# Kernel optimization log

Measured on AMD Instinct MI355X. Metric: run time of the kernel, lower is better.

## Reference

```python
import jax, jax.numpy as jnp
import numpy as np
from functools import partial

NODES = 50
IN_SZ = 12
HID = 6


def _conv(x, W, b):
    # x: [N, C, H, W], W: [O, I, 3, 3], pad 1 -> same H, W
    y = jax.lax.conv_general_dilated(x, W, window_strides=(1, 1),
                                     padding=((1, 1), (1, 1)),
                                     dimension_numbers=('NCHW', 'OIHW', 'NCHW'))
    return y + b[None, :, None, None]


def setup_inputs() -> dict:
    key = jax.random.key(0)
    ks = jax.random.split(key, 12)
    B, T = 4096, 12
    d = {}
    d['A_hat'] = jax.random.normal(ks[0], (NODES, NODES), dtype=jnp.float32)
    d['X'] = jax.random.normal(ks[1], (B, NODES, T, IN_SZ, 1), dtype=jnp.float32)
    s_ih = 1.0 / np.sqrt(HID)
    d['W_ih'] = jax.random.uniform(ks[2], (4 * HID, IN_SZ), jnp.float32, -s_ih, s_ih)
    d['W_hh'] = jax.random.uniform(ks[3], (4 * HID, HID), jnp.float32, -s_ih, s_ih)
    d['b_ih'] = jax.random.uniform(ks[4], (4 * HID,), jnp.float32, -s_ih, s_ih)
    d['b_hh'] = jax.random.uniform(ks[5], (4 * HID,), jnp.float32, -s_ih, s_ih)
    d['Wf1'] = jax.random.normal(ks[6], (100, 50, 3, 3), jnp.float32) * 0.05
    d['bf1'] = jnp.zeros((100,), jnp.float32)
    d['Wf2'] = jax.random.normal(ks[7], (100, 100, 3, 3), jnp.float32) * 0.05
    d['bf2'] = jnp.zeros((100,), jnp.float32)
    d['Wf3'] = jax.random.normal(ks[8], (50, 100, 3, 3), jnp.float32) * 0.05
    d['bf3'] = jnp.zeros((50,), jnp.float32)
    d['W_lean'] = jax.random.normal(ks[9], (HID, HID), jnp.float32) * 0.3
    d['b_lean'] = jnp.zeros((HID,), jnp.float32)
    return d


def reference(A_hat, X, W_ih, W_hh, b_ih, b_hh, Wf1, bf1, Wf2, bf2, Wf3, bf3, W_lean, b_lean):
    # out1: [S, 50, 12] with S = B*T; the Python loop over S becomes a scan
    out1 = jnp.squeeze(X, axis=4).reshape(-1, NODES, IN_SZ)

    def step(carry, x_t):
        h, c = carry  # each [50, 6]
        gates = x_t @ W_ih.T + b_ih + h @ W_hh.T + b_hh  # [50, 24]
        i, f, g, o = jnp.split(gates, 4, axis=-1)
        i = jax.nn.sigmoid(i)
        f = jax.nn.sigmoid(f)
        g = jnp.tanh(g)
        o = jax.nn.sigmoid(o)
        c_new = f * c + i * g
        h_new = o * jnp.tanh(c_new)
        h_new = jnp.tanh(h_new)  # module applies extra tanh and feeds it back
        return (h_new, c_new), h_new

    h0 = jnp.zeros((NODES, HID), dtype=X.dtype)
    c0 = jnp.zeros((NODES, HID), dtype=X.dtype)
    _, al = jax.lax.scan(step, (h0, c0), out1)  # al: [S, 50, 6]

    out2 = al.reshape(-1, NODES, HID, 1)  # [S, 50, 6, 1]
    f = jax.nn.relu(_conv(out2, Wf1, bf1))
    f = jax.nn.relu(_conv(f, Wf2, bf2))
    f = jax.nn.relu(_conv(f, Wf3, bf3))
    out = (f.reshape(-1, HID) @ W_lean.T + b_lean).reshape(-1, NODES, HID, 1)
    return out
```

## Files before the change

kernel.cpp:

```cpp
#include <hip/hip_runtime.h>

#define NCH 1024
#define CL 48
#define WM 24

typedef _Float16 half8 __attribute__((ext_vector_type(8)));
typedef float f32x4 __attribute__((ext_vector_type(4)));

#define ROWB 256
#define BUFB 17408

__device__ __forceinline__ int swz(int srow, int b){ return srow*ROWB + (b ^ ((srow&7)<<4)); }

__device__ __forceinline__ unsigned short f2h_bits(float x){
  _Float16 h = (_Float16)x;
  return __builtin_bit_cast(unsigned short, h);
}

__device__ __forceinline__ float rcp_(float x){ return __builtin_amdgcn_rcpf(x); }
__device__ __forceinline__ float tanh_(float z){ return 1.f - 2.f*rcp_(1.f + __expf(2.f*z)); }

__global__ void pack_frags(const float* __restrict__ W1, const float* __restrict__ W2,
                           const float* __restrict__ W3, unsigned short* __restrict__ ws)
{
  int tid = blockIdx.x*256 + threadIdx.x;
  if (tid >= 174*512) return;
  int f = tid >> 9, e = tid & 511, l = e >> 3, j = e & 7;
  int d, ks, nt, I, O; const float* W;
  if (f < 42)      { int x = f;     int st = x/7;  nt = x%7; d = st/2; ks = st%2; I = 50;  O = 100; W = W1; }
  else if (f < 126){ int x = f-42;  int st = x/7;  nt = x%7; d = st/4; ks = st%4; I = 100; O = 100; W = W2; }
  else             { int x = f-126; int st = x/4;  nt = x%4; d = st/4; ks = st%4; I = 100; O = 50;  W = W3; }
  int k = ks*32 + ((l>>4)<<3) + j;
  int o = nt*16 + (l&15);
  float v = (k < I && o < O) ? W[((o*I + k)*3 + d)*3 + 1] : 0.f;
  ws[tid] = f2h_bits(v);
}

__global__ __launch_bounds__(64,3) void lstm_scan(
    const float* __restrict__ X, const float* __restrict__ Wih,
    const float* __restrict__ Whh, const float* __restrict__ bih,
    const float* __restrict__ bhh, float* __restrict__ al)
{
  const int l = threadIdx.x;
  const int blk = blockIdx.x;
  const int chunk = blk / 5, w = blk - chunk*5;
  const int q = l / 6, j = l - q*6;
  const bool active = (q < 10);
  const int n = w*10 + (active ? q : 0);
  const int sbase = active ? q*6 : 0;

  const int s_begin = chunk * CL;
  const int s_start = (s_begin >= WM) ? (s_begin - WM) : 0;
  const int s_end   = s_begin + CL;

  float wi[4][12], wh[4][6], bb[4];
  #pragma unroll
  for (int g=0; g<4; ++g){
    const int r = g*6 + j;
    const float4 w0 = *(const float4*)(Wih + r*12);
    const float4 w1 = *(const float4*)(Wih + r*12 + 4);
    const float4 w2 = *(const float4*)(Wih + r*12 + 8);
    wi[g][0]=w0.x; wi[g][1]=w0.y; wi[g][2]=w0.z; wi[g][3]=w0.w;
    wi[g][4]=w1.x; wi[g][5]=w1.y; wi[g][6]=w1.z; wi[g][7]=w1.w;
    wi[g][8]=w2.x; wi[g][9]=w2.y; wi[g][10]=w2.z; wi[g][11]=w2.w;
    const float2 h0 = *(const float2*)(Whh + r*6);
    const float2 h1 = *(const float2*)(Whh + r*6 + 2);
    const float2 h2 = *(const float2*)(Whh + r*6 + 4);
    wh[g][0]=h0.x; wh[g][1]=h0.y; wh[g][2]=h1.x;
    wh[g][3]=h1.y; wh[g][4]=h2.x; wh[g][5]=h2.y;
    bb[g] = bih[r] + bhh[r];
  }

  float h[6];
  #pragma unroll
  for (int k=0;k<6;++k) h[k] = 0.f;
  float c = 0.f;

  const float* xp = X + (size_t)s_start*600 + n*12;
  float4 xa = ((const float4*)xp)[0];
  float4 xb = ((const float4*)xp)[1];
  float4 xc = ((const float4*)xp)[2];

  for (int s = s_start; s < s_end; ++s){
    const float xr[12] = {xa.x,xa.y,xa.z,xa.w, xb.x,xb.y,xb.z,xb.w,
                          xc.x,xc.y,xc.z,xc.w};
    const int sn = (s+1 < s_end) ? (s+1) : s;
    const float* xq = X + (size_t)sn*600 + n*12;
    const float4 ya = ((const float4*)xq)[0];
    const float4 yb = ((const float4*)xq)[1];
    const float4 yc = ((const float4*)xq)[2];

    float a0 = bb[0], a1 = bb[1], a2 = bb[2], a3 = bb[3];
    #pragma unroll
    for (int k=0;k<12;++k){
      a0 += wi[0][k]*xr[k]; a1 += wi[1][k]*xr[k];
      a2 += wi[2][k]*xr[k]; a3 += wi[3][k]*xr[k];
    }
    #pragma unroll
    for (int k=0;k<6;++k){
      a0 += wh[0][k]*h[k]; a1 += wh[1][k]*h[k];
      a2 += wh[2][k]*h[k]; a3 += wh[3][k]*h[k];
    }
    const float gi = rcp_(1.f + __expf(-a0));
    const float gf = rcp_(1.f + __expf(-a1));
    const float gg = 2.f*rcp_(1.f + __expf(-(a2+a2))) - 1.f;
    const float go = rcp_(1.f + __expf(-a3));
    c = gf*c + gi*gg;
    const float hn = tanh_(go * tanh_(c));

    if (active && s >= s_begin) al[(size_t)s*300 + n*6 + j] = hn;

    #pragma unroll
    for (int k=0;k<6;++k) h[k] = __shfl(hn, sbase + k, 64);

    xa = ya; xb = yb; xc = yc;
  }
}

template<int KS, int NTT, int NTG, bool LAST>
__device__ __forceinline__ void conv_layer2(
    char* lds, int inOff, int outOff, const unsigned short* __restrict__ wsU,
    int fbase, int ntOff, const float* __restrict__ bias, int O, int m0, int lane)
{
  f32x4 acc[2][NTG];
  #pragma unroll
  for (int m=0;m<2;m++)
    #pragma unroll
    for (int n=0;n<NTG;n++) acc[m][n] = (f32x4){0.f,0.f,0.f,0.f};

  const int ar = m0 + (lane & 15);
  const int abyte_g = (lane>>4)<<4;
  const int laneb = lane << 3;

  half8 a0c = *(const half8*)(lds + inOff + swz(ar, abyte_g));
  half8 a1c = *(const half8*)(lds + inOff + swz(ar + 16, abyte_g));
  half8 bc[NTG];
  {
    const unsigned short* p0 = wsU + (size_t)(fbase + ntOff)*512 + laneb;
    #pragma unroll
    for (int n=0;n<NTG;n++) bc[n] = *(const half8*)(p0 + n*512);
  }

  #pragma unroll
  for (int st=0; st<3*KS; ++st){
    half8 a0n, a1n, bn[NTG];
    if (st+1 < 3*KS){
      const int dn = (st+1)/KS, ksn = (st+1)%KS;
      a0n = *(const half8*)(lds + inOff + swz(ar + dn, ksn*64 + abyte_g));
      a1n = *(const half8*)(lds + inOff + swz(ar + 16 + dn, ksn*64 + abyte_g));
      const unsigned short* pn = wsU + (size_t)(fbase + (st+1)*NTT + ntOff)*512 + laneb;
      #pragma unroll
      for (int n=0;n<NTG;n++) bn[n] = *(const half8*)(pn + n*512);
    }
    #pragma unroll
    for (int n=0;n<NTG;n++){
      acc[0][n] = __builtin_amdgcn_mfma_f32_16x16x32_f16(a0c, bc[n], acc[0][n], 0, 0, 0);
      acc[1][n] = __builtin_amdgcn_mfma_f32_16x16x32_f16(a1c, bc[n], acc[1][n], 0, 0, 0);
    }
    if (st+1 < 3*KS){
      a0c = a0n; a1c = a1n;
      #pragma unroll
      for (int n=0;n<NTG;n++) bc[n] = bn[n];
    }
  }

  const int colBase = lane & 15;
  #pragma unroll
  for (int m=0;m<2;m++){
    const int rbase = m0 + m*16 + ((lane>>4)<<2);
    #pragma unroll
    for (int n=0;n<NTG;n++){
      const int col = (ntOff + n)*16 + colBase;
      if (col < O){
        const float b = bias[col];
        #pragma unroll
        for (int r=0;r<4;r++){
          const int crow = rbase + r;
          const int p8 = crow & 7;
          if (p8 >= 1 && p8 <= 6){
            const float v = fmaxf(acc[m][n][r] + b, 0.f);
            const int srow = crow + 1;
            if (LAST) *(float*)(lds + outOff + swz(srow, col*4)) = v;
            else      *(unsigned short*)(lds + outOff + swz(srow, col*2)) = f2h_bits(v);
          }
        }
      }
    }
  }
}

__global__ __launch_bounds__(256,4) void conv_mfma_kernel(
    float* __restrict__ io, const unsigned short* __restrict__ wsU,
    const float* __restrict__ b1, const float* __restrict__ b2, const float* __restrict__ b3,
    const float* __restrict__ Wl, const float* __restrict__ bl)
{
  __shared__ __align__(16) char lds[2*BUFB];
  const int t = threadIdx.x;
  const int lane = t & 63, w = t >> 6;
  const int mg = w >> 1, ng = w & 1;
  const int m0 = mg*32;
  const size_t base = (size_t)blockIdx.x * 2400;

  for (int i = t; i < (2*BUFB)/16; i += 256) ((f32x4*)lds)[i] = (f32x4){0.f,0.f,0.f,0.f};
  __syncthreads();

  for (int idx = t; idx < 2400; idx += 256){
    const float v = io[base + idx];
    const int s = idx/300, rr = idx%300;
    const int ch = rr/6, y = rr%6;
    *(unsigned short*)(lds + swz(s*8 + y + 2, ch*2)) = f2h_bits(v);
  }
  __syncthreads();

  if (ng == 0) conv_layer2<2,7,4,false>(lds, 0,    BUFB, wsU, 0,   0, b1, 100, m0, lane);
  else         conv_layer2<2,7,3,false>(lds, 0,    BUFB, wsU, 0,   4, b1, 100, m0, lane);
  __syncthreads();
  if (ng == 0) conv_layer2<4,7,4,false>(lds, BUFB, 0,    wsU, 42,  0, b2, 100, m0, lane);
  else         conv_layer2<4,7,3,false>(lds, BUFB, 0,    wsU, 42,  4, b2, 100, m0, lane);
  __syncthreads();
  if (ng == 0) conv_layer2<4,4,2,true >(lds, 0,    BUFB, wsU, 126, 0, b3, 50,  m0, lane);
  else         conv_layer2<4,4,2,true >(lds, 0,    BUFB, wsU, 126, 2, b3, 50,  m0, lane);
  __syncthreads();

  for (int idx = t; idx < 2400; idx += 256){
    const int s = idx/300, rr = idx%300;
    const int n = rr/6, j = rr%6;
    float sum = bl[j];
    #pragma unroll
    for (int y=0; y<6; y++)
      sum += Wl[j*6+y] * (*(const float*)(lds + BUFB + swz(s*8 + y + 2, n*4)));
    io[base + idx] = sum;
  }
}

__device__ __forceinline__ float wraw(const float* __restrict__ W, int I, int i, int d, int o){
  return W[((o*I + i)*3 + d)*3 + 1];
}
template<int NS>
__device__ void conv_layer_valu(const float (* __restrict__ in)[100][8],
                                float (* __restrict__ outb)[100][8],
                                int I, const float* __restrict__ W,
                                const float* __restrict__ bias, int o, int s0)
{
  float acc[NS][6];
  const float b = bias[o];
  #pragma unroll
  for (int s=0;s<NS;s++)
    #pragma unroll
    for (int y=0;y<6;y++) acc[s][y]=b;
  for (int i=0;i<I;i++){
    const float w0 = wraw(W,I,i,0,o), w1 = wraw(W,I,i,1,o), w2 = wraw(W,I,i,2,o);
    #pragma unroll
    for (int s=0;s<NS;s++){
      const float4 r0 = *(const float4*)&in[s0+s][i][0];
      const float4 r1 = *(const float4*)&in[s0+s][i][4];
      acc[s][0] += w1*r0.x + w2*r0.y;
      acc[s][1] += w0*r0.x + w1*r0.y + w2*r0.z;
      acc[s][2] += w0*r0.y + w1*r0.z + w2*r0.w;
      acc[s][3] += w0*r0.z + w1*r0.w + w2*r1.x;
      acc[s][4] += w0*r0.w + w1*r1.x + w2*r1.y;
      acc[s][5] += w0*r1.x + w1*r1.y;
    }
  }
  #pragma unroll
  for (int s=0;s<NS;s++){
    float4 v0; float2 v1;
    v0.x = fmaxf(acc[s][0],0.f); v0.y = fmaxf(acc[s][1],0.f);
    v0.z = fmaxf(acc[s][2],0.f); v0.w = fmaxf(acc[s][3],0.f);
    v1.x = fmaxf(acc[s][4],0.f); v1.y = fmaxf(acc[s][5],0.f);
    *(float4*)&outb[s0+s][o][0] = v0;
    *(float2*)&outb[s0+s][o][4] = v1;
  }
}
__global__ __launch_bounds__(256,1) void conv_kernel_fb(
    float* __restrict__ io,
    const float* __restrict__ W1, const float* __restrict__ b1,
    const float* __restrict__ W2, const float* __restrict__ b2,
    const float* __restrict__ W3, const float* __restrict__ b3,
    const float* __restrict__ Wl, const float* __restrict__ bl)
{
  __shared__ float A[8][100][8];
  __shared__ float B[8][100][8];
  const int t = threadIdx.x;
  const size_t base = (size_t)blockIdx.x * 2400;
  for (int idx=t; idx<800; idx+=256){
    const int s = idx/100, ch = idx%100;
    A[s][ch][6]=0.f; A[s][ch][7]=0.f; B[s][ch][6]=0.f; B[s][ch][7]=0.f;
  }
  for (int idx=t; idx<2400; idx+=256){
    const float v = io[base + idx];
    const int s = idx/300, rr = idx%300;
    A[s][rr/6][rr%6] = v;
  }
  __syncthreads();
  const int w = t>>6, lane = t&63;
  { const int sh = w>>1, o = (w&1)*50 + lane;
    if (lane < 50) conv_layer_valu<4>(A, B, 50, W1, b1, o, sh*4); }
  __syncthreads();
  { const int sh = w>>1, o = (w&1)*50 + lane;
    if (lane < 50) conv_layer_valu<4>(B, A, 100, W2, b2, o, sh*4); }
  __syncthreads();
  { if (lane < 50) conv_layer_valu<2>(A, B, 100, W3, b3, lane, w*2); }
  __syncthreads();
  for (int idx=t; idx<2400; idx+=256){
    const int s = idx/300, rr = idx%300, n = rr/6, j = rr%6;
    const float4 r0 = *(const float4*)&B[s][n][0];
    const float2 r1 = *(const float2*)&B[s][n][4];
    io[base + idx] = bl[j] + Wl[j*6+0]*r0.x + Wl[j*6+1]*r0.y + Wl[j*6+2]*r0.z
                   + Wl[j*6+3]*r0.w + Wl[j*6+4]*r1.x + Wl[j*6+5]*r1.y;
  }
}

extern "C" void kernel_launch(void* const* d_in, const int* in_sizes, int n_in,
                              void* d_out, int out_size, void* d_ws, size_t ws_size,
                              hipStream_t stream)
{
  const float* X    = (const float*)d_in[1];
  const float* Wih  = (const float*)d_in[2];
  const float* Whh  = (const float*)d_in[3];
  const float* bih  = (const float*)d_in[4];
  const float* bhh  = (const float*)d_in[5];
  const float* Wf1  = (const float*)d_in[6];
  const float* bf1  = (const float*)d_in[7];
  const float* Wf2  = (const float*)d_in[8];
  const float* bf2  = (const float*)d_in[9];
  const float* Wf3  = (const float*)d_in[10];
  const float* bf3  = (const float*)d_in[11];
  const float* Wl   = (const float*)d_in[12];
  const float* bl   = (const float*)d_in[13];
  float* out = (float*)d_out;

  const bool packed = (ws_size >= 174*512*sizeof(unsigned short));
  if (packed)
    hipLaunchKernelGGL(pack_frags, dim3(348), dim3(256), 0, stream,
                       Wf1, Wf2, Wf3, (unsigned short*)d_ws);

  hipLaunchKernelGGL(lstm_scan, dim3(NCH*5), dim3(64), 0, stream,
                     X, Wih, Whh, bih, bhh, out);

  if (packed)
    hipLaunchKernelGGL(conv_mfma_kernel, dim3(6144), dim3(256), 0, stream,
                       out, (const unsigned short*)d_ws, bf1, bf2, bf3, Wl, bl);
  else
    hipLaunchKernelGGL(conv_kernel_fb, dim3(6144), dim3(256), 0, stream,
                       out, Wf1, bf1, Wf2, bf2, Wf3, bf3, Wl, bl);
}
```

Baseline: 215.5 us.

## Interleave two LSTM chunks per wave and pass hidden states as fp16

Each LSTM wave now runs two independent sequence chunks interleaved, which halves the grid and gives the latency-bound recurrence two independent dependency chains to overlap. The LSTM output is written as fp16 into workspace and the conv kernel reads it directly, which halves the intermediate traffic and removes the conversion in the conv load. The risks are fewer waves in flight for the LSTM and more registers per thread. It also depends on a large workspace being available; otherwise it falls back to fp32.

```diff
diff --git a/kernel.cpp b/kernel.cpp
--- a/kernel.cpp
+++ b/kernel.cpp
@@ -9,6 +9,7 @@
 
 #define ROWB 256
 #define BUFB 17408
+#define ALH_OFF 131072
 
 __device__ __forceinline__ int swz(int srow, int b){ return srow*ROWB + (b ^ ((srow&7)<<4)); }
 
@@ -36,22 +37,23 @@
   ws[tid] = f2h_bits(v);
 }
 
-__global__ __launch_bounds__(64,3) void lstm_scan(
+template<bool F16>
+__global__ __launch_bounds__(64,3) void lstm_scan2(
     const float* __restrict__ X, const float* __restrict__ Wih,
     const float* __restrict__ Whh, const float* __restrict__ bih,
-    const float* __restrict__ bhh, float* __restrict__ al)
+    const float* __restrict__ bhh, float* __restrict__ al32,
+    unsigned short* __restrict__ al16)
 {
   const int l = threadIdx.x;
   const int blk = blockIdx.x;
-  const int chunk = blk / 5, w = blk - chunk*5;
-  const int q = l / 6, j = l - q*6;
+  const int p = blk/5, w = blk - p*5;
+  const int q = l/6, j = l - q*6;
   const bool active = (q < 10);
   const int n = w*10 + (active ? q : 0);
   const int sbase = active ? q*6 : 0;
 
-  const int s_begin = chunk * CL;
-  const int s_start = (s_begin >= WM) ? (s_begin - WM) : 0;
-  const int s_end   = s_begin + CL;
+  const int sAb = 2*p*CL, sBb = sAb + CL;
+  const int sALast = sAb + CL - 1, sBLast = sBb + CL - 1;
 
   float wi[4][12], wh[4][6], bb[4];
   #pragma unroll
@@ -71,49 +73,64 @@
     bb[g] = bih[r] + bhh[r];
   }
 
-  float h[6];
-  #pragma unroll
-  for (int k=0;k<6;++k) h[k] = 0.f;
-  float c = 0.f;
-
-  const float* xp = X + (size_t)s_start*600 + n*12;
-  float4 xa = ((const float4*)xp)[0];
-  float4 xb = ((const float4*)xp)[1];
-  float4 xc = ((const float4*)xp)[2];
-
-  for (int s = s_start; s < s_end; ++s){
-    const float xr[12] = {xa.x,xa.y,xa.z,xa.w, xb.x,xb.y,xb.z,xb.w,
-                          xc.x,xc.y,xc.z,xc.w};
-    const int sn = (s+1 < s_end) ? (s+1) : s;
-    const float* xq = X + (size_t)sn*600 + n*12;
-    const float4 ya = ((const float4*)xq)[0];
-    const float4 yb = ((const float4*)xq)[1];
-    const float4 yc = ((const float4*)xq)[2];
-
-    float a0 = bb[0], a1 = bb[1], a2 = bb[2], a3 = bb[3];
-    #pragma unroll
-    for (int k=0;k<12;++k){
-      a0 += wi[0][k]*xr[k]; a1 += wi[1][k]*xr[k];
-      a2 += wi[2][k]*xr[k]; a3 += wi[3][k]*xr[k];
-    }
-    #pragma unroll
-    for (int k=0;k<6;++k){
-      a0 += wh[0][k]*h[k]; a1 += wh[1][k]*h[k];
-      a2 += wh[2][k]*h[k]; a3 += wh[3][k]*h[k];
-    }
+  float hA[6], hB[6], cA = 0.f, cB = 0.f;
+  #pragma unroll
+  for (int k=0;k<6;++k){ hA[k]=0.f; hB[k]=0.f; }
+
+  const int sA0 = (p==0) ? 0 : (sAb - WM);
+  const int sB0 = sBb - WM;
+  float4 xA0,xA1,xA2, xB0,xB1,xB2;
+  { const float4* pa = (const float4*)(X + (size_t)sA0*600 + n*12); xA0=pa[0]; xA1=pa[1]; xA2=pa[2]; }
+  { const float4* pb = (const float4*)(X + (size_t)sB0*600 + n*12); xB0=pb[0]; xB1=pb[1]; xB2=pb[2]; }
+
+  auto step = [&](const float4& x0, const float4& x1, const float4& x2,
+                  float* h, float& c) -> float {
+    const float xr[12] = {x0.x,x0.y,x0.z,x0.w, x1.x,x1.y,x1.z,x1.w, x2.x,x2.y,x2.z,x2.w};
+    float a0=bb[0], a1=bb[1], a2=bb[2], a3=bb[3];
+    #pragma unroll
+    for (int k=0;k<12;++k){ a0+=wi[0][k]*xr[k]; a1+=wi[1][k]*xr[k];
+                            a2+=wi[2][k]*xr[k]; a3+=wi[3][k]*xr[k]; }
+    #pragma unroll
+    for (int k=0;k<6;++k){ a0+=wh[0][k]*h[k]; a1+=wh[1][k]*h[k];
+                           a2+=wh[2][k]*h[k]; a3+=wh[3][k]*h[k]; }
     const float gi = rcp_(1.f + __expf(-a0));
     const float gf = rcp_(1.f + __expf(-a1));
     const float gg = 2.f*rcp_(1.f + __expf(-(a2+a2))) - 1.f;
     const float go = rcp_(1.f + __expf(-a3));
     c = gf*c + gi*gg;
-    const float hn = tanh_(go * tanh_(c));
-
-    if (active && s >= s_begin) al[(size_t)s*300 + n*6 + j] = hn;
-
-    #pragma unroll
-    for (int k=0;k<6;++k) h[k] = __shfl(hn, sbase + k, 64);
-
-    xa = ya; xb = yb; xc = yc;
+    return tanh_(go * tanh_(c));
+  };
+
+  for (int i = -WM; i < CL; ++i){
+    const int sA = sAb + i, sB = sBb + i;
+    const bool doA = (sA >= 0);
+    float4 yA0,yA1,yA2, yB0,yB1,yB2;
+    { const int sn = (sB < sBLast) ? sB+1 : sBLast;
+      const float4* xq = (const float4*)(X + (size_t)sn*600 + n*12);
+      yB0=xq[0]; yB1=xq[1]; yB2=xq[2]; }
+    if (doA){
+      const int sn = (sA < sALast) ? sA+1 : sALast;
+      const float4* xq = (const float4*)(X + (size_t)sn*600 + n*12);
+      yA0=xq[0]; yA1=xq[1]; yA2=xq[2];
+    }
+
+    float hnA = 0.f;
+    if (doA) hnA = step(xA0,xA1,xA2, hA, cA);
+    const float hnB = step(xB0,xB1,xB2, hB, cB);
+
+    if (active && i >= 0){
+      const size_t oA = (size_t)sA*300 + n*6 + j;
+      const size_t oB = (size_t)sB*300 + n*6 + j;
+      if (F16){ al16[oA] = f2h_bits(hnA); al16[oB] = f2h_bits(hnB); }
+      else    { al32[oA] = hnA;           al32[oB] = hnB; }
+    }
+    #pragma unroll
+    for (int k=0;k<6;++k){
+      hA[k] = __shfl(hnA, sbase + k, 64);
+      hB[k] = __shfl(hnB, sbase + k, 64);
+    }
+    if (doA){ xA0=yA0; xA1=yA1; xA2=yA2; }
+    xB0=yB0; xB1=yB1; xB2=yB2;
   }
 }
 
@@ -189,8 +206,10 @@
   }
 }
 
+template<bool ALH>
 __global__ __launch_bounds__(256,4) void conv_mfma_kernel(
-    float* __restrict__ io, const unsigned short* __restrict__ wsU,
+    float* __restrict__ io, const unsigned short* __restrict__ alh,
+    const unsigned short* __restrict__ wsU,
     const float* __restrict__ b1, const float* __restrict__ b2, const float* __restrict__ b3,
     const float* __restrict__ Wl, const float* __restrict__ bl)
 {
@@ -204,11 +223,23 @@
   for (int i = t; i < (2*BUFB)/16; i += 256) ((f32x4*)lds)[i] = (f32x4){0.f,0.f,0.f,0.f};
   __syncthreads();
 
-  for (int idx = t; idx < 2400; idx += 256){
-    const float v = io[base + idx];
-    const int s = idx/300, rr = idx%300;
-    const int ch = rr/6, y = rr%6;
-    *(unsigned short*)(lds + swz(s*8 + y + 2, ch*2)) = f2h_bits(v);
+  if (ALH){
+    const unsigned short* ap = alh + base;
+    for (int idx = t; idx < 400; idx += 256){
+      const int s = idx/50, n = idx - (idx/50)*50;
+      const unsigned short* pp = ap + s*300 + n*6;
+      const int r0 = s*8 + 2;
+      #pragma unroll
+      for (int y=0; y<6; ++y)
+        *(unsigned short*)(lds + swz(r0 + y, n*2)) = pp[y];
+    }
+  } else {
+    for (int idx = t; idx < 2400; idx += 256){
+      const float v = io[base + idx];
+      const int s = idx/300, rr = idx%300;
+      const int ch = rr/6, y = rr%6;
+      *(unsigned short*)(lds + swz(s*8 + y + 2, ch*2)) = f2h_bits(v);
+    }
   }
   __syncthreads();
 
@@ -329,19 +360,29 @@
   const float* Wl   = (const float*)d_in[12];
   const float* bl   = (const float*)d_in[13];
   float* out = (float*)d_out;
+  unsigned short* wsU = (unsigned short*)d_ws;
 
   const bool packed = (ws_size >= 174*512*sizeof(unsigned short));
+  const bool bigws  = (ws_size >= (size_t)(ALH_OFF + 49152ull*300ull)*2ull);
+
   if (packed)
     hipLaunchKernelGGL(pack_frags, dim3(348), dim3(256), 0, stream,
-                       Wf1, Wf2, Wf3, (unsigned short*)d_ws);
-
-  hipLaunchKernelGGL(lstm_scan, dim3(NCH*5), dim3(64), 0, stream,
-                     X, Wih, Whh, bih, bhh, out);
-
-  if (packed)
-    hipLaunchKernelGGL(conv_mfma_kernel, dim3(6144), dim3(256), 0, stream,
-                       out, (const unsigned short*)d_ws, bf1, bf2, bf3, Wl, bl);
-  else
-    hipLaunchKernelGGL(conv_kernel_fb, dim3(6144), dim3(256), 0, stream,
-                       out, Wf1, bf1, Wf2, bf2, Wf3, bf3, Wl, bl);
-}
+                       Wf1, Wf2, Wf3, wsU);
+
+  if (bigws && packed){
+    unsigned short* alh = wsU + ALH_OFF;
+    hipLaunchKernelGGL((lstm_scan2<true>), dim3((NCH/2)*5), dim3(64), 0, stream,
+                       X, Wih, Whh, bih, bhh, nullptr, alh);
+    hipLaunchKernelGGL((conv_mfma_kernel<true>), dim3(6144), dim3(256), 0, stream,
+                       out, alh, wsU, bf1, bf2, bf3, Wl, bl);
+  } else {
+    hipLaunchKernelGGL((lstm_scan2<false>), dim3((NCH/2)*5), dim3(64), 0, stream,
+                       X, Wih, Whh, bih, bhh, out, nullptr);
+    if (packed)
+      hipLaunchKernelGGL((conv_mfma_kernel<false>), dim3(6144), dim3(256), 0, stream,
+                         out, nullptr, wsU, bf1, bf2, bf3, Wl, bl);
+    else
+      hipLaunchKernelGGL(conv_kernel_fb, dim3(6144), dim3(256), 0, stream,
+                         out, Wf1, bf1, Wf2, bf2, Wf3, bf3, Wl, bl);
+  }
+}
```

New measurement: 217.7 us. Within noise of the previous version (+1.0%).
